# Performance work log

Measured on AMD Instinct MI355X. Metric: run time of the kernel, lower is better.

## Reference

```python
import jax, jax.numpy as jnp
import numpy as np

N_EMBEDDINGS = 1024
EMBEDDING_DIM = 256
DECAY = 0.99
EPSILON = 1e-05


def setup_inputs() -> dict:
    key = jax.random.key(0)
    k1, k2, k3 = jax.random.split(key, 3)
    inputs = jax.random.normal(k1, (16, 64, 64, EMBEDDING_DIM), dtype=jnp.float32)
    codebook = jax.random.normal(k2, (N_EMBEDDINGS, EMBEDDING_DIM), dtype=jnp.float32)
    ema_w = jax.random.normal(k3, (N_EMBEDDINGS, EMBEDDING_DIM), dtype=jnp.float32)
    ema_cluster_size = jnp.zeros((N_EMBEDDINGS,), dtype=jnp.float32)
    return {"inputs": inputs, "codebook": codebook, "ema_w": ema_w,
            "ema_cluster_size": ema_cluster_size}


def reference(inputs, codebook, ema_w, ema_cluster_size):
    input_shape = inputs.shape
    flat = inputs.reshape(-1, EMBEDDING_DIM)  # [N, D]
    # Squared Euclidean pairwise distances: [N, K]
    dists = (jnp.sum(flat * flat, axis=1, keepdims=True)
             + jnp.sum(codebook * codebook, axis=1)[None, :]
             - 2.0 * flat @ codebook.T)
    idx = jnp.argmin(dists, axis=1)  # [N]
    encodings = jax.nn.one_hot(idx, N_EMBEDDINGS, dtype=flat.dtype)  # [N, K]
    quantized = (encodings @ codebook).reshape(input_shape)
    # EMA updates (training mode)
    cs = ema_cluster_size * DECAY + (1.0 - DECAY) * jnp.sum(encodings, axis=0)
    n = jnp.sum(cs)
    cs = (cs + EPSILON) / (n + cs * EPSILON) * n  # faithful to original expression
    dw = encodings.T @ flat  # [K, D] scatter-accumulate via matmul
    new_ema_w = ema_w * DECAY + (1.0 - DECAY) * dw
    new_codebook = new_ema_w / cs[:, None]
    return quantized, encodings, cs, new_ema_w, new_codebook
```

## Files before the change

### kernel.cpp

```cpp
#include <hip/hip_runtime.h>

#define N_ROWS 65536
#define D 256
#define K 1024
#define DECAYF 0.99f
#define OMDF 0.01f
#define EPSF 1e-5f

typedef _Float16 f16;
typedef _Float16 f16x8 __attribute__((ext_vector_type(8)));
typedef float f32x16 __attribute__((ext_vector_type(16)));
typedef float f32x4 __attribute__((ext_vector_type(4)));

__global__ __launch_bounds__(256) void prep_kernel(const float* __restrict__ cb,
                                                   float* __restrict__ cnorm,
                                                   char* __restrict__ wsB,
                                                   float* __restrict__ dw,
                                                   float* __restrict__ counts) {
    const int tid = threadIdx.x;
    const int bid = blockIdx.x;
    const int g = bid * 256 + tid;
    *reinterpret_cast<float4*>(dw + (size_t)g * 4) = make_float4(0.f, 0.f, 0.f, 0.f);
    if (g < K) counts[g] = 0.f;
    {
        const int row = bid * 4 + (tid >> 6);
        const int lane = tid & 63;
        const float4 v = *reinterpret_cast<const float4*>(cb + (size_t)row * D + lane * 4);
        float s = v.x * v.x + v.y * v.y + v.z * v.z + v.w * v.w;
        #pragma unroll
        for (int m = 32; m; m >>= 1) s += __shfl_xor(s, m);
        if (lane == 0) cnorm[row] = s;
    }
    {
        const int sp = g & 15;
        const int c = (g >> 4) & 255;
        const int sd = g >> 12;
        const int ct = sd >> 2, dk = sd & 3;
        const int sl = sp ^ (c & 15);
        const int v = sl >> 3, ks = (sl >> 1) & 3, h = sl & 1;
        const float* src = cb + (size_t)(ct * 256 + c) * D + dk * 64 + ks * 16 + h * 8;
        f16 out[8];
        #pragma unroll
        for (int e = 0; e < 8; ++e) {
            const float f = src[e];
            const f16 hi = (f16)f;
            out[e] = v ? (f16)(f - (float)hi) : hi;
        }
        *reinterpret_cast<f16x8*>(wsB + (size_t)g * 16) = *reinterpret_cast<f16x8*>(out);
    }
}

__global__ __launch_bounds__(256, 2) void argmin_mfma_kernel(
        const float* __restrict__ x, const char* __restrict__ wsB,
        const float* __restrict__ cnorm, int* __restrict__ idx_out,
        float* __restrict__ counts) {
    __shared__ char smem[81920];
    char* Alds = smem;
    char* Blds = smem + 16384;
    const int tid = threadIdx.x;
    const int wave = tid >> 6;
    const int lane = tid & 63;
    const int rw = wave >> 1;
    const int cw = wave & 1;
    const int l31 = lane & 31;
    const int h = lane >> 5;
    const int n0 = blockIdx.x * 64;

    float bestv[16];
    int besti[16];
    #pragma unroll
    for (int r = 0; r < 16; ++r) { bestv[r] = 3.4e38f; besti[r] = 0; }

    const int s_row = tid >> 2;
    const int s_c4 = tid & 3;

    for (int ct = 0; ct < 4; ++ct) {
        f32x16 acc[4];
        #pragma unroll
        for (int cf = 0; cf < 4; ++cf)
            #pragma unroll
            for (int r = 0; r < 16; ++r) acc[cf][r] = 0.f;

        for (int dks = 0; dks < 4; ++dks) {
            const int dk = (ct & 1) ? (3 - dks) : dks;
            __syncthreads();
            if (!(ct > 0 && dks == 0)) {
                const float4* xs = reinterpret_cast<const float4*>(
                    x + (size_t)(n0 + s_row) * D + dk * 64 + s_c4 * 16);
                float f[16];
                {
                    const float4 f0 = xs[0], f1 = xs[1], f2 = xs[2], f3 = xs[3];
                    f[0]=f0.x; f[1]=f0.y; f[2]=f0.z; f[3]=f0.w;
                    f[4]=f1.x; f[5]=f1.y; f[6]=f1.z; f[7]=f1.w;
                    f[8]=f2.x; f[9]=f2.y; f[10]=f2.z; f[11]=f2.w;
                    f[12]=f3.x; f[13]=f3.y; f[14]=f3.z; f[15]=f3.w;
                }
                f16 hi[16], lo[16];
                #pragma unroll
                for (int e = 0; e < 16; ++e) {
                    hi[e] = (f16)f[e];
                    lo[e] = (f16)(f[e] - (float)hi[e]);
                }
                const int sw = s_row & 15;
                char* Abase = Alds + s_row * 256;
                *reinterpret_cast<f16x8*>(Abase + (((s_c4 * 2 + 0) ^ sw) * 16)) = *reinterpret_cast<f16x8*>(&hi[0]);
                *reinterpret_cast<f16x8*>(Abase + (((s_c4 * 2 + 1) ^ sw) * 16)) = *reinterpret_cast<f16x8*>(&hi[8]);
                *reinterpret_cast<f16x8*>(Abase + (((8 + s_c4 * 2 + 0) ^ sw) * 16)) = *reinterpret_cast<f16x8*>(&lo[0]);
                *reinterpret_cast<f16x8*>(Abase + (((8 + s_c4 * 2 + 1) ^ sw) * 16)) = *reinterpret_cast<f16x8*>(&lo[8]);
            }
            {
                const int4* gsrc = reinterpret_cast<const int4*>(wsB + ((size_t)(ct * 4 + dk) << 16));
                int4* ldst = reinterpret_cast<int4*>(Blds);
                #pragma unroll
                for (int i = 0; i < 16; ++i) ldst[tid + i * 256] = gsrc[tid + i * 256];
            }
            __syncthreads();
            const int arow = rw * 32 + l31;
            const int asw = arow & 15;
            #pragma unroll
            for (int ks = 0; ks < 4; ++ks) {
                const int sA = ks * 2 + h;
                const f16x8 Ah = *reinterpret_cast<const f16x8*>(Alds + arow * 256 + ((sA ^ asw) * 16));
                const f16x8 Al = *reinterpret_cast<const f16x8*>(Alds + arow * 256 + (((8 + sA) ^ asw) * 16));
                #pragma unroll
                for (int cf = 0; cf < 4; ++cf) {
                    const int bcode = cw * 128 + cf * 32 + l31;
                    const char* Bbase = Blds + bcode * 256;
                    const int bsw = bcode & 15;
                    const f16x8 Bh = *reinterpret_cast<const f16x8*>(Bbase + ((sA ^ bsw) * 16));
                    const f16x8 Bl = *reinterpret_cast<const f16x8*>(Bbase + (((8 + sA) ^ bsw) * 16));
                    acc[cf] = __builtin_amdgcn_mfma_f32_32x32x16_f16(Ah, Bh, acc[cf], 0, 0, 0);
                    acc[cf] = __builtin_amdgcn_mfma_f32_32x32x16_f16(Ah, Bl, acc[cf], 0, 0, 0);
                    acc[cf] = __builtin_amdgcn_mfma_f32_32x32x16_f16(Al, Bh, acc[cf], 0, 0, 0);
                }
            }
        }
        #pragma unroll
        for (int cf = 0; cf < 4; ++cf) {
            const int code = ct * 256 + cw * 128 + cf * 32 + l31;
            const float cn = cnorm[code];
            #pragma unroll
            for (int r = 0; r < 16; ++r) {
                const float dist = cn - 2.f * acc[cf][r];
                if (dist < bestv[r]) { bestv[r] = dist; besti[r] = code; }
            }
        }
    }
    #pragma unroll
    for (int r = 0; r < 16; ++r) {
        float v = bestv[r];
        int b = besti[r];
        #pragma unroll
        for (int m = 16; m; m >>= 1) {
            const float ov = __shfl_xor(v, m);
            const int ob = __shfl_xor(b, m);
            if (ov < v || (ov == v && ob < b)) { v = ov; b = ob; }
        }
        bestv[r] = v; besti[r] = b;
    }
    __syncthreads();
    float* Sv = reinterpret_cast<float*>(smem);
    int*   Si = reinterpret_cast<int*>(smem + 512);
    if (l31 == 0) {
        #pragma unroll
        for (int r = 0; r < 16; ++r) {
            const int row = rw * 32 + (r & 3) + 8 * (r >> 2) + 4 * h;
            Sv[cw * 64 + row] = bestv[r];
            Si[cw * 64 + row] = besti[r];
        }
    }
    __syncthreads();
    if (tid < 64) {
        const float v0 = Sv[tid], v1 = Sv[64 + tid];
        const int b0 = Si[tid], b1 = Si[64 + tid];
        const bool take1 = (v1 < v0) || (v1 == v0 && b1 < b0);
        const int b = take1 ? b1 : b0;
        idx_out[n0 + tid] = b;
        atomicAdd(&counts[b], 1.0f);
    }
}

__global__ __launch_bounds__(256) void quant_kernel(const float* __restrict__ cb,
                                                    const int* __restrict__ idx,
                                                    float* __restrict__ quant) {
    const int n = blockIdx.x * 4 + (threadIdx.x >> 6);
    const int lane = threadIdx.x & 63;
    const int i = idx[n];
    const f32x4 c = *reinterpret_cast<const f32x4*>(cb + (size_t)i * D + lane * 4);
    __builtin_nontemporal_store(c, reinterpret_cast<f32x4*>(quant + (size_t)n * D + lane * 4));
}

__global__ __launch_bounds__(256) void enc_kernel(const int* __restrict__ idx,
                                                  float* __restrict__ enc) {
    const int total = N_ROWS * (K / 4);
    for (int g = blockIdx.x * blockDim.x + threadIdx.x; g < total;
         g += gridDim.x * blockDim.x) {
        const int n = g >> 8;
        const int k0 = (g & 255) * 4;
        const int i = idx[n];
        f32x4 v;
        v[0] = (k0 == i) ? 1.f : 0.f;
        v[1] = (k0 + 1 == i) ? 1.f : 0.f;
        v[2] = (k0 + 2 == i) ? 1.f : 0.f;
        v[3] = (k0 + 3 == i) ? 1.f : 0.f;
        __builtin_nontemporal_store(v, reinterpret_cast<f32x4*>(enc + (size_t)g * 4));
    }
}

__global__ __launch_bounds__(1024) void cs_scan_kernel(const float* __restrict__ ema_cs,
                                                       const float* __restrict__ counts,
                                                       float* __restrict__ cs_out,
                                                       int* __restrict__ cursor) {
    __shared__ float wsum[16];
    __shared__ int wisum[16];
    __shared__ float n_sh;
    const int k = threadIdx.x;
    const int wid = k >> 6;
    const int lane = k & 63;
    const float cnt = counts[k];
    const float c = ema_cs[k] * DECAYF + OMDF * cnt;
    const int ic = (int)cnt;
    int v = ic;
    #pragma unroll
    for (int d = 1; d < 64; d <<= 1) {
        const int t = __shfl_up(v, d);
        if (lane >= d) v += t;
    }
    float s = c;
    #pragma unroll
    for (int m = 32; m; m >>= 1) s += __shfl_xor(s, m);
    if (lane == 63) wisum[wid] = v;
    if (lane == 0) wsum[wid] = s;
    __syncthreads();
    if (k == 0) {
        float n = 0.f;
        for (int w = 0; w < 16; ++w) n += wsum[w];
        n_sh = n;
    }
    if (wid == 0 && lane < 16) {
        int wv = wisum[lane];
        #pragma unroll
        for (int d = 1; d < 16; d <<= 1) {
            const int t = __shfl_up(wv, d);
            if (lane >= d) wv += t;
        }
        wisum[lane] = wv;
    }
    __syncthreads();
    const float n = n_sh;
    cs_out[k] = (c + EPSF) / (n + c * EPSF) * n;
    const int wbase = (wid == 0) ? 0 : wisum[wid - 1];
    cursor[k] = wbase + v - ic;
}

__global__ __launch_bounds__(256) void scatter_kernel(const int* __restrict__ idx,
                                                      int* __restrict__ cursor,
                                                      int* __restrict__ rowlist,
                                                      int* __restrict__ codelist) {
    const int n = blockIdx.x * 256 + threadIdx.x;
    const int i = idx[n];
    const int pos = atomicAdd(&cursor[i], 1);
    rowlist[pos] = n;
    codelist[pos] = i;
}

__global__ __launch_bounds__(256) void chunk_sum_kernel(const float* __restrict__ x,
                                                        const int* __restrict__ rowlist,
                                                        const int* __restrict__ codelist,
                                                        float* __restrict__ dw) {
    const int wave = threadIdx.x >> 6;
    const int lane = threadIdx.x & 63;
    const int p0 = blockIdx.x * 32 + wave * 8;
    int rows[8], codes[8];
    #pragma unroll
    for (int j = 0; j < 8; ++j) {
        rows[j] = rowlist[p0 + j];
        codes[j] = codelist[p0 + j];
    }
    float4 v[8];
    #pragma unroll
    for (int j = 0; j < 8; ++j)
        v[j] = *reinterpret_cast<const float4*>(x + (size_t)rows[j] * D + lane * 4);
    float4 s = v[0];
    int cur = codes[0];
    #pragma unroll
    for (int j = 1; j < 8; ++j) {
        if (codes[j] != cur) {
            float* dst = dw + (size_t)cur * D + lane * 4;
            atomicAdd(dst + 0, s.x); atomicAdd(dst + 1, s.y);
            atomicAdd(dst + 2, s.z); atomicAdd(dst + 3, s.w);
            cur = codes[j];
            s = v[j];
        } else {
            s.x += v[j].x; s.y += v[j].y; s.z += v[j].z; s.w += v[j].w;
        }
    }
    float* dst = dw + (size_t)cur * D + lane * 4;
    atomicAdd(dst + 0, s.x); atomicAdd(dst + 1, s.y);
    atomicAdd(dst + 2, s.z); atomicAdd(dst + 3, s.w);
}

__global__ __launch_bounds__(256) void ema_kernel(const float* __restrict__ ema_w,
                                                  const float* __restrict__ dw,
                                                  const float* __restrict__ cs,
                                                  float* __restrict__ w_out,
                                                  float* __restrict__ cb_out) {
    const int e4 = blockIdx.x * blockDim.x + threadIdx.x;
    const int k = e4 >> 6;
    const float csk = cs[k];
    const float4 w = *reinterpret_cast<const float4*>(ema_w + (size_t)e4 * 4);
    const float4 d = *reinterpret_cast<const float4*>(dw + (size_t)e4 * 4);
    float4 nw, nc;
    nw.x = w.x * DECAYF + OMDF * d.x;
    nw.y = w.y * DECAYF + OMDF * d.y;
    nw.z = w.z * DECAYF + OMDF * d.z;
    nw.w = w.w * DECAYF + OMDF * d.w;
    nc.x = nw.x / csk; nc.y = nw.y / csk; nc.z = nw.z / csk; nc.w = nw.w / csk;
    *reinterpret_cast<float4*>(w_out + (size_t)e4 * 4) = nw;
    *reinterpret_cast<float4*>(cb_out + (size_t)e4 * 4) = nc;
}

extern "C" void kernel_launch(void* const* d_in, const int* in_sizes, int n_in,
                              void* d_out, int out_size, void* d_ws, size_t ws_size,
                              hipStream_t stream) {
    (void)in_sizes; (void)n_in; (void)out_size; (void)ws_size;
    const float* x      = (const float*)d_in[0];
    const float* cb     = (const float*)d_in[1];
    const float* ema_w  = (const float*)d_in[2];
    const float* ema_cs = (const float*)d_in[3];

    float* out    = (float*)d_out;
    float* quant  = out;
    float* enc    = quant + 16777216;
    float* cs_out = enc + 67108864;
    float* w_out  = cs_out + 1024;
    float* cb_out = w_out + 262144;

    float* ws       = (float*)d_ws;
    float* counts   = ws;
    float* dw       = ws + 1024;
    float* cnorm    = ws + 263168;
    int*   cursor   = (int*)(ws + 264192);
    int*   idx      = (int*)(ws + 265216);
    int*   rowlist  = (int*)(ws + 330752);
    int*   codelist = (int*)(ws + 396288);
    char*  wsB      = (char*)(ws + 461824);

    prep_kernel<<<256, 256, 0, stream>>>(cb, cnorm, wsB, dw, counts);
    argmin_mfma_kernel<<<N_ROWS / 64, 256, 0, stream>>>(x, wsB, cnorm, idx, counts);
    quant_kernel<<<N_ROWS / 4, 256, 0, stream>>>(cb, idx, quant);
    enc_kernel<<<2048, 256, 0, stream>>>(idx, enc);
    cs_scan_kernel<<<1, 1024, 0, stream>>>(ema_cs, counts, cs_out, cursor);
    scatter_kernel<<<N_ROWS / 256, 256, 0, stream>>>(idx, cursor, rowlist, codelist);
    chunk_sum_kernel<<<2048, 256, 0, stream>>>(x, rowlist, codelist, dw);
    ema_kernel<<<65536 / 256, 256, 0, stream>>>(ema_w, dw, cs_out, w_out, cb_out);
}
```

Before: 336.1 us.

## Stage full input tile in LDS and stream codebook fragments from global

The argmin kernel now converts the whole 64x256 input tile to split-f16 in LDS once. It drops the per-chunk B staging through LDS and loads pre-laid-out codebook fragments directly from global memory in MFMA register order. Each of the four waves now owns 64 codes across all 64 rows, and the prep kernel rewrites the codebook layout to match. The scatter kernel also aggregates per-block histograms in shared memory, so it issues one global atomic per code instead of one per row. This removes per-step block syncs and LDS B traffic, at the cost of relying on L2/global bandwidth for B reads.

```diff
diff --git a/kernel.cpp b/kernel.cpp
--- a/kernel.cpp
+++ b/kernel.cpp
@@ -32,13 +32,16 @@
         if (lane == 0) cnorm[row] = s;
     }
     {
-        const int sp = g & 15;
-        const int c = (g >> 4) & 255;
-        const int sd = g >> 12;
-        const int ct = sd >> 2, dk = sd & 3;
-        const int sl = sp ^ (c & 15);
-        const int v = sl >> 3, ks = (sl >> 1) & 3, h = sl & 1;
-        const float* src = cb + (size_t)(ct * 256 + c) * D + dk * 64 + ks * 16 + h * 8;
+        const int l31 = g & 31;
+        const int h   = (g >> 5) & 1;
+        const int cfg = (g >> 6) & 7;
+        const int v   = (g >> 9) & 1;
+        const int ks  = (g >> 10) & 3;
+        const int dk  = (g >> 12) & 3;
+        const int ct  = (g >> 14) & 3;
+        const int code = ct * 256 + cfg * 32 + l31;
+        const int dim0 = dk * 64 + ks * 16 + h * 8;
+        const float* src = cb + (size_t)code * D + dim0;
         f16 out[8];
         #pragma unroll
         for (int e = 0; e < 8; ++e) {
@@ -54,127 +57,145 @@
         const float* __restrict__ x, const char* __restrict__ wsB,
         const float* __restrict__ cnorm, int* __restrict__ idx_out,
         float* __restrict__ counts) {
-    __shared__ char smem[81920];
-    char* Alds = smem;
-    char* Blds = smem + 16384;
+    __shared__ char smem[67584];
     const int tid = threadIdx.x;
-    const int wave = tid >> 6;
+    const int cw = tid >> 6;
     const int lane = tid & 63;
-    const int rw = wave >> 1;
-    const int cw = wave & 1;
     const int l31 = lane & 31;
     const int h = lane >> 5;
     const int n0 = blockIdx.x * 64;
 
-    float bestv[16];
-    int besti[16];
-    #pragma unroll
-    for (int r = 0; r < 16; ++r) { bestv[r] = 3.4e38f; besti[r] = 0; }
-
-    const int s_row = tid >> 2;
-    const int s_c4 = tid & 3;
-
+    {
+        const int s_row = tid >> 2;
+        const int c4 = tid & 3;
+        const float4* src = reinterpret_cast<const float4*>(
+            x + (size_t)(n0 + s_row) * D + c4 * 64);
+        char* rowbase = smem + s_row * 1024;
+        const int sw = s_row & 7;
+        #pragma unroll
+        for (int j = 0; j < 8; ++j) {
+            const float4 f0 = src[j * 2];
+            const float4 f1 = src[j * 2 + 1];
+            float f[8] = {f0.x, f0.y, f0.z, f0.w, f1.x, f1.y, f1.z, f1.w};
+            f16 hi8[8], lo8[8];
+            #pragma unroll
+            for (int e = 0; e < 8; ++e) {
+                hi8[e] = (f16)f[e];
+                lo8[e] = (f16)(f[e] - (float)hi8[e]);
+            }
+            const int ph = (c4 * 8 + j) ^ sw;
+            *reinterpret_cast<f16x8*>(rowbase + ph * 16)       = *reinterpret_cast<f16x8*>(hi8);
+            *reinterpret_cast<f16x8*>(rowbase + 512 + ph * 16) = *reinterpret_cast<f16x8*>(lo8);
+        }
+    }
+    __syncthreads();
+
+    float bestv[2][16];
+    int besti[2][16];
+    #pragma unroll
+    for (int rf = 0; rf < 2; ++rf)
+        #pragma unroll
+        for (int r = 0; r < 16; ++r) { bestv[rf][r] = 3.4e38f; besti[rf][r] = 0; }
+
+    const int lane16 = lane * 16;
+    const int arow0 = l31;
+    const int arow1 = 32 + l31;
+    char* abase0 = smem + arow0 * 1024;
+    char* abase1 = smem + arow1 * 1024;
+    const int asw0 = arow0 & 7;
+    const int asw1 = arow1 & 7;
+    const int cfg0 = cw * 2;
+
+    #pragma unroll 1
     for (int ct = 0; ct < 4; ++ct) {
-        f32x16 acc[4];
-        #pragma unroll
-        for (int cf = 0; cf < 4; ++cf)
-            #pragma unroll
-            for (int r = 0; r < 16; ++r) acc[cf][r] = 0.f;
-
-        for (int dks = 0; dks < 4; ++dks) {
-            const int dk = (ct & 1) ? (3 - dks) : dks;
-            __syncthreads();
-            if (!(ct > 0 && dks == 0)) {
-                const float4* xs = reinterpret_cast<const float4*>(
-                    x + (size_t)(n0 + s_row) * D + dk * 64 + s_c4 * 16);
-                float f[16];
-                {
-                    const float4 f0 = xs[0], f1 = xs[1], f2 = xs[2], f3 = xs[3];
-                    f[0]=f0.x; f[1]=f0.y; f[2]=f0.z; f[3]=f0.w;
-                    f[4]=f1.x; f[5]=f1.y; f[6]=f1.z; f[7]=f1.w;
-                    f[8]=f2.x; f[9]=f2.y; f[10]=f2.z; f[11]=f2.w;
-                    f[12]=f3.x; f[13]=f3.y; f[14]=f3.z; f[15]=f3.w;
-                }
-                f16 hi[16], lo[16];
+        f32x16 acc[2][2];
+        #pragma unroll
+        for (int rf = 0; rf < 2; ++rf)
+            #pragma unroll
+            for (int cf = 0; cf < 2; ++cf)
                 #pragma unroll
-                for (int e = 0; e < 16; ++e) {
-                    hi[e] = (f16)f[e];
-                    lo[e] = (f16)(f[e] - (float)hi[e]);
-                }
-                const int sw = s_row & 15;
-                char* Abase = Alds + s_row * 256;
-                *reinterpret_cast<f16x8*>(Abase + (((s_c4 * 2 + 0) ^ sw) * 16)) = *reinterpret_cast<f16x8*>(&hi[0]);
-                *reinterpret_cast<f16x8*>(Abase + (((s_c4 * 2 + 1) ^ sw) * 16)) = *reinterpret_cast<f16x8*>(&hi[8]);
-                *reinterpret_cast<f16x8*>(Abase + (((8 + s_c4 * 2 + 0) ^ sw) * 16)) = *reinterpret_cast<f16x8*>(&lo[0]);
-                *reinterpret_cast<f16x8*>(Abase + (((8 + s_c4 * 2 + 1) ^ sw) * 16)) = *reinterpret_cast<f16x8*>(&lo[8]);
-            }
-            {
-                const int4* gsrc = reinterpret_cast<const int4*>(wsB + ((size_t)(ct * 4 + dk) << 16));
-                int4* ldst = reinterpret_cast<int4*>(Blds);
-                #pragma unroll
-                for (int i = 0; i < 16; ++i) ldst[tid + i * 256] = gsrc[tid + i * 256];
-            }
-            __syncthreads();
-            const int arow = rw * 32 + l31;
-            const int asw = arow & 15;
+                for (int r = 0; r < 16; ++r) acc[rf][cf][r] = 0.f;
+
+        #pragma unroll
+        for (int dk = 0; dk < 4; ++dk) {
             #pragma unroll
             for (int ks = 0; ks < 4; ++ks) {
-                const int sA = ks * 2 + h;
-                const f16x8 Ah = *reinterpret_cast<const f16x8*>(Alds + arow * 256 + ((sA ^ asw) * 16));
-                const f16x8 Al = *reinterpret_cast<const f16x8*>(Alds + arow * 256 + (((8 + sA) ^ asw) * 16));
-                #pragma unroll
-                for (int cf = 0; cf < 4; ++cf) {
-                    const int bcode = cw * 128 + cf * 32 + l31;
-                    const char* Bbase = Blds + bcode * 256;
-                    const int bsw = bcode & 15;
-                    const f16x8 Bh = *reinterpret_cast<const f16x8*>(Bbase + ((sA ^ bsw) * 16));
-                    const f16x8 Bl = *reinterpret_cast<const f16x8*>(Bbase + (((8 + sA) ^ bsw) * 16));
-                    acc[cf] = __builtin_amdgcn_mfma_f32_32x32x16_f16(Ah, Bh, acc[cf], 0, 0, 0);
-                    acc[cf] = __builtin_amdgcn_mfma_f32_32x32x16_f16(Ah, Bl, acc[cf], 0, 0, 0);
-                    acc[cf] = __builtin_amdgcn_mfma_f32_32x32x16_f16(Al, Bh, acc[cf], 0, 0, 0);
-                }
-            }
-        }
-        #pragma unroll
-        for (int cf = 0; cf < 4; ++cf) {
-            const int code = ct * 256 + cw * 128 + cf * 32 + l31;
-            const float cn = cnorm[code];
+                const int sbase = (((ct * 4 + dk) * 4 + ks) * 2) * 8;
+                const f16x8 B00 = *reinterpret_cast<const f16x8*>(wsB + (size_t)(sbase + cfg0 + 0) * 1024 + lane16);
+                const f16x8 B10 = *reinterpret_cast<const f16x8*>(wsB + (size_t)(sbase + cfg0 + 1) * 1024 + lane16);
+                const f16x8 B01 = *reinterpret_cast<const f16x8*>(wsB + (size_t)(sbase + 8 + cfg0 + 0) * 1024 + lane16);
+                const f16x8 B11 = *reinterpret_cast<const f16x8*>(wsB + (size_t)(sbase + 8 + cfg0 + 1) * 1024 + lane16);
+                const int g = dk * 8 + ks * 2 + h;
+                const f16x8 Ah0 = *reinterpret_cast<const f16x8*>(abase0 + ((g ^ asw0) * 16));
+                const f16x8 Al0 = *reinterpret_cast<const f16x8*>(abase0 + 512 + ((g ^ asw0) * 16));
+                const f16x8 Ah1 = *reinterpret_cast<const f16x8*>(abase1 + ((g ^ asw1) * 16));
+                const f16x8 Al1 = *reinterpret_cast<const f16x8*>(abase1 + 512 + ((g ^ asw1) * 16));
+                acc[0][0] = __builtin_amdgcn_mfma_f32_32x32x16_f16(Ah0, B00, acc[0][0], 0, 0, 0);
+                acc[0][0] = __builtin_amdgcn_mfma_f32_32x32x16_f16(Ah0, B01, acc[0][0], 0, 0, 0);
+                acc[0][0] = __builtin_amdgcn_mfma_f32_32x32x16_f16(Al0, B00, acc[0][0], 0, 0, 0);
+                acc[0][1] = __builtin_amdgcn_mfma_f32_32x32x16_f16(Ah0, B10, acc[0][1], 0, 0, 0);
+                acc[0][1] = __builtin_amdgcn_mfma_f32_32x32x16_f16(Ah0, B11, acc[0][1], 0, 0, 0);
+                acc[0][1] = __builtin_amdgcn_mfma_f32_32x32x16_f16(Al0, B10, acc[0][1], 0, 0, 0);
+                acc[1][0] = __builtin_amdgcn_mfma_f32_32x32x16_f16(Ah1, B00, acc[1][0], 0, 0, 0);
+                acc[1][0] = __builtin_amdgcn_mfma_f32_32x32x16_f16(Ah1, B01, acc[1][0], 0, 0, 0);
+                acc[1][0] = __builtin_amdgcn_mfma_f32_32x32x16_f16(Al1, B00, acc[1][0], 0, 0, 0);
+                acc[1][1] = __builtin_amdgcn_mfma_f32_32x32x16_f16(Ah1, B10, acc[1][1], 0, 0, 0);
+                acc[1][1] = __builtin_amdgcn_mfma_f32_32x32x16_f16(Ah1, B11, acc[1][1], 0, 0, 0);
+                acc[1][1] = __builtin_amdgcn_mfma_f32_32x32x16_f16(Al1, B10, acc[1][1], 0, 0, 0);
+            }
+        }
+        const int code0 = ct * 256 + cw * 64 + l31;
+        const int code1 = code0 + 32;
+        const float cn0 = cnorm[code0];
+        const float cn1 = cnorm[code1];
+        #pragma unroll
+        for (int rf = 0; rf < 2; ++rf)
             #pragma unroll
             for (int r = 0; r < 16; ++r) {
-                const float dist = cn - 2.f * acc[cf][r];
-                if (dist < bestv[r]) { bestv[r] = dist; besti[r] = code; }
-            }
-        }
-    }
-    #pragma unroll
-    for (int r = 0; r < 16; ++r) {
-        float v = bestv[r];
-        int b = besti[r];
-        #pragma unroll
-        for (int m = 16; m; m >>= 1) {
-            const float ov = __shfl_xor(v, m);
-            const int ob = __shfl_xor(b, m);
+                const float d0 = cn0 - 2.f * acc[rf][0][r];
+                const float d1 = cn1 - 2.f * acc[rf][1][r];
+                float dv = d0; int db = code0;
+                if (d1 < dv) { dv = d1; db = code1; }
+                if (dv < bestv[rf][r]) { bestv[rf][r] = dv; besti[rf][r] = db; }
+            }
+    }
+    #pragma unroll
+    for (int rf = 0; rf < 2; ++rf)
+        #pragma unroll
+        for (int r = 0; r < 16; ++r) {
+            float v = bestv[rf][r];
+            int b = besti[rf][r];
+            #pragma unroll
+            for (int m = 16; m; m >>= 1) {
+                const float ov = __shfl_xor(v, m);
+                const int ob = __shfl_xor(b, m);
+                if (ov < v || (ov == v && ob < b)) { v = ov; b = ob; }
+            }
+            bestv[rf][r] = v; besti[rf][r] = b;
+        }
+    __syncthreads();
+    float* Sv = reinterpret_cast<float*>(smem + 65536);
+    int*   Si = reinterpret_cast<int*>(smem + 66560);
+    if (l31 == 0) {
+        #pragma unroll
+        for (int rf = 0; rf < 2; ++rf)
+            #pragma unroll
+            for (int r = 0; r < 16; ++r) {
+                const int row = rf * 32 + (r & 3) + 8 * (r >> 2) + 4 * h;
+                Sv[cw * 64 + row] = bestv[rf][r];
+                Si[cw * 64 + row] = besti[rf][r];
+            }
+    }
+    __syncthreads();
+    if (tid < 64) {
+        float v = Sv[tid];
+        int b = Si[tid];
+        #pragma unroll
+        for (int w = 1; w < 4; ++w) {
+            const float ov = Sv[w * 64 + tid];
+            const int ob = Si[w * 64 + tid];
             if (ov < v || (ov == v && ob < b)) { v = ov; b = ob; }
         }
-        bestv[r] = v; besti[r] = b;
-    }
-    __syncthreads();
-    float* Sv = reinterpret_cast<float*>(smem);
-    int*   Si = reinterpret_cast<int*>(smem + 512);
-    if (l31 == 0) {
-        #pragma unroll
-        for (int r = 0; r < 16; ++r) {
-            const int row = rw * 32 + (r & 3) + 8 * (r >> 2) + 4 * h;
-            Sv[cw * 64 + row] = bestv[r];
-            Si[cw * 64 + row] = besti[r];
-        }
-    }
-    __syncthreads();
-    if (tid < 64) {
-        const float v0 = Sv[tid], v1 = Sv[64 + tid];
-        const int b0 = Si[tid], b1 = Si[64 + tid];
-        const bool take1 = (v1 < v0) || (v1 == v0 && b1 < b0);
-        const int b = take1 ? b1 : b0;
         idx_out[n0 + tid] = b;
         atomicAdd(&counts[b], 1.0f);
     }
@@ -257,9 +278,23 @@
                                                       int* __restrict__ cursor,
                                                       int* __restrict__ rowlist,
                                                       int* __restrict__ codelist) {
-    const int n = blockIdx.x * 256 + threadIdx.x;
+    __shared__ int hist[1024];
+    const int tid = threadIdx.x;
+    #pragma unroll
+    for (int j = 0; j < 4; ++j) hist[tid + j * 256] = 0;
+    __syncthreads();
+    const int n = blockIdx.x * 256 + tid;
     const int i = idx[n];
-    const int pos = atomicAdd(&cursor[i], 1);
+    atomicAdd(&hist[i], 1);
+    __syncthreads();
+    #pragma unroll
+    for (int j = 0; j < 4; ++j) {
+        const int k = tid + j * 256;
+        const int c = hist[k];
+        hist[k] = (c > 0) ? atomicAdd(&cursor[k], c) : 0;
+    }
+    __syncthreads();
+    const int pos = atomicAdd(&hist[i], 1);
     rowlist[pos] = n;
     codelist[pos] = i;
 }
```

Measured after the change: 394.2 us. +17.3%, slower.
